# Kernel tuning notes

Measured on AMD Instinct MI355X. Metric: run time of the kernel, lower is better.

Reference implementation:

```python
import jax, jax.numpy as jnp
import numpy as np

L = 4          # GAT_LAYERS
HEADS = 4      # N_HEADS
H = 64         # transformer hidden dim
DH = H // HEADS
FIN = 32       # NODE_EMBED_SIZE
A = 15         # gats.num_actions (readout size)
OBS = 1500     # flattened obs dim
HS = 512       # hidden_size (policy FC)
NOUT = 15      # num_outputs
VH = 128       # VALUE_HIDDENS
B = 128        # batch of graphs
N = 1000       # nodes per map graph
TOT = B * N
DEG = 4
E = TOT * DEG


def _lin(key, fan_in, shape):
    return jax.random.normal(key, shape, jnp.float32) * (1.0 / np.sqrt(fan_in))


def setup_inputs() -> dict:
    key = jax.random.key(0)
    ks = jax.random.split(key, 30)
    node_feats = jax.random.normal(ks[0], (TOT, FIN), jnp.float32)
    obs = jax.random.normal(ks[1], (B, OBS), jnp.float32)
    # batched-graph edges: endpoints stay within each graph (DGL batch semantics)
    off = (jnp.arange(B) * N)[:, None]
    edge_src = (jax.random.randint(ks[2], (B, N * DEG), 0, N) + off).reshape(-1).astype(jnp.int32)
    edge_dst = (jax.random.randint(ks[3], (B, N * DEG), 0, N) + off).reshape(-1).astype(jnp.int32)
    agent_nodes = (jax.random.randint(ks[4], (B,), 0, N) + jnp.arange(B) * N).astype(jnp.int32)
    p = {
        'W_in': _lin(ks[5], FIN, (FIN, H)),
        'Wq': _lin(ks[6], H, (L, H, H)), 'Wk': _lin(ks[7], H, (L, H, H)),
        'Wv': _lin(ks[8], H, (L, H, H)), 'Wo': _lin(ks[9], H, (L, H, H)),
        'ln1_g': jnp.ones((L, H), jnp.float32), 'ln1_b': jnp.zeros((L, H), jnp.float32),
        'W1': _lin(ks[10], H, (L, H, 2 * H)), 'b1': jnp.zeros((L, 2 * H), jnp.float32),
        'W2': _lin(ks[11], 2 * H, (L, 2 * H, H)), 'b2': jnp.zeros((L, H), jnp.float32),
        'ln2_g': jnp.ones((L, H), jnp.float32), 'ln2_b': jnp.zeros((L, H), jnp.float32),
        'Wr': _lin(ks[12], H, (H, A)), 'br': jnp.zeros((A,), jnp.float32),
        'Wp1': _lin(ks[13], A + OBS, (A + OBS, HS)), 'bp1': jnp.zeros((HS,), jnp.float32),
        'Wp2': _lin(ks[14], HS, (HS, HS)), 'bp2': jnp.zeros((HS,), jnp.float32),
        'Wlog': _lin(ks[15], HS, (HS, NOUT)), 'blog': jnp.zeros((NOUT,), jnp.float32),
        'Wv1': _lin(ks[16], OBS, (OBS, VH)), 'bv1': jnp.zeros((VH,), jnp.float32),
        'Wv2': _lin(ks[17], VH, (VH, VH)), 'bv2': jnp.zeros((VH,), jnp.float32),
        'Wvo': _lin(ks[18], VH, (VH, 1)), 'bvo': jnp.zeros((1,), jnp.float32),
    }
    return dict(node_feats=node_feats, obs=obs, edge_src=edge_src, edge_dst=edge_dst,
                agent_nodes=agent_nodes, **p)


def _layernorm(x, g, b):
    m = x.mean(-1, keepdims=True)
    v = ((x - m) ** 2).mean(-1, keepdims=True)
    return (x - m) * jax.lax.rsqrt(v + 1e-5) * g + b


def reference(node_feats, obs, edge_src, edge_dst, agent_nodes, W_in, Wq, Wk, Wv, Wo,
              ln1_g, ln1_b, W1, b1, W2, b2, ln2_g, ln2_b, Wr, br,
              Wp1, bp1, Wp2, bp2, Wlog, blog, Wv1, bv1, Wv2, bv2, Wvo, bvo):
    n = node_feats.shape[0]
    x = node_feats @ W_in                                   # [n, H]
    inv_sqrt_dh = np.float32(1.0 / np.sqrt(DH))
    for l in range(L):
        q = (x @ Wq[l]).reshape(n, HEADS, DH)
        k = (x @ Wk[l]).reshape(n, HEADS, DH)
        v = (x @ Wv[l]).reshape(n, HEADS, DH)
        # per-edge attention scores, softmax over incoming edges of each dst node
        s = jnp.sum(q[edge_dst] * k[edge_src], axis=-1) * inv_sqrt_dh   # [E, HEADS]
        m = jax.ops.segment_max(s, edge_dst, num_segments=n)            # [n, HEADS]
        w = jnp.exp(s - m[edge_dst])
        denom = jax.ops.segment_sum(w, edge_dst, num_segments=n)        # [n, HEADS]
        agg = jax.ops.segment_sum(w[:, :, None] * v[edge_src], edge_dst, num_segments=n)
        attn = (agg / (denom[:, :, None] + 1e-9)).reshape(n, H) @ Wo[l]
        x = _layernorm(x + attn, ln1_g[l], ln1_b[l])
        h = jax.nn.relu(x @ W1[l] + b1[l]) @ W2[l] + b2[l]
        x = _layernorm(x + h, ln2_g[l], ln2_b[l])
    gat_out = x[agent_nodes] @ Wr + br                      # [B, A] per-agent action features
    feat = jnp.tanh(jnp.concatenate([gat_out, obs], axis=1) @ Wp1 + bp1)
    feat = jnp.tanh(feat @ Wp2 + bp2)
    logits = feat @ Wlog + blog                             # [B, NOUT]
    vh = jnp.tanh(obs @ Wv1 + bv1)
    vh = jnp.tanh(vh @ Wv2 + bv2)
    value = (vh @ Wvo + bvo)[:, 0]                          # [B]
    return logits, value
```

## Files before the change

kernel.cpp:

```cpp
#include <hip/hip_runtime.h>
#include <hip/hip_bf16.h>
#include <cstdint>
#include <cstddef>

#define DEV static __device__ __forceinline__

constexpr int GRAPHS = 128;
constexpr int NPG    = 1000;
constexpr int EPG    = 4000;
constexpr int TOTN   = GRAPHS * NPG;
constexpr int TOTE   = GRAPHS * EPG;
constexpr int HD     = 64;
constexpr int OBSD   = 1500;
constexpr int AD     = 15;

typedef __attribute__((ext_vector_type(8))) short bf16x8;
typedef __attribute__((ext_vector_type(4))) float f32x4;

DEV unsigned short f2b(float f){
  unsigned u = __float_as_uint(f);
  return (unsigned short)((u + 0x7fffu + ((u >> 16) & 1u)) >> 16);
}
DEV float b2f(unsigned short s){ return __uint_as_float((unsigned)s << 16); }

// ... 69 lines not shown
  int e = blockIdx.x*256 + threadIdx.x;
  int pos = atomicAdd(&cursor[edst[e]], 1);
  esorted[pos] = esrc[e];
}

__global__ __launch_bounds__(256) void k_in(const float* __restrict__ nf,
                                            const float* __restrict__ Win,
                                            unsigned short* __restrict__ xb){
  __shared__ float  s_nf[256*36];
  __shared__ float4 s_w[512];
  const int tid = threadIdx.x;
  const int node0 = blockIdx.x * 256;
  const float4* W4 = (const float4*)Win;
  s_w[tid] = W4[tid]; s_w[tid+256] = W4[tid+256];
  const float4* nf4 = (const float4*)nf;
  float4* snf4 = (float4*)s_nf;
  #pragma unroll
  for (int r=0;r<8;r++){
    int i = tid + 256*r; int n = i>>3, k4 = i&7;
    snf4[n*9 + k4] = nf4[(size_t)(node0+n)*8 + k4];
  }
  __syncthreads();
  const int ng = tid>>2, cg = tid&3;
  float4 acc[4][4];
  #pragma unroll
  for (int i=0;i<4;i++){ acc[i][0]=make_float4(0,0,0,0); acc[i][1]=make_float4(0,0,0,0);
                         acc[i][2]=make_float4(0,0,0,0); acc[i][3]=make_float4(0,0,0,0); }
  #pragma unroll 4
  for (int k=0;k<32;k++){
    float nv[4];
    #pragma unroll
    for (int i=0;i<4;i++) nv[i] = s_nf[(ng + 64*i)*36 + k];
    float4 w[4];
    #pragma unroll
    for (int j=0;j<4;j++) w[j] = s_w[k*16 + cg*4 + j];
    #pragma unroll
    for (int i=0;i<4;i++){
      #pragma unroll
      for (int j=0;j<4;j++) fma4(acc[i][j], nv[i], w[j]);
    }
  }
  ushort4* xb4 = (ushort4*)xb;
  #pragma unroll
  for (int i=0;i<4;i++){
    size_t nidx = (size_t)(node0 + ng + 64*i) * 16;
    #pragma unroll
    for (int j=0;j<4;j++) xb4[nidx + cg*4 + j] = pack4(acc[i][j]);
  }
}

__global__ __launch_bounds__(256) void k_qkv_m(const unsigned short* __restrict__ xb,
    const unsigned short* __restrict__ wqkvT,
    unsigned short* __restrict__ qkv){
  __shared__ short s_w[192*72];
  __shared__ short s_st[4][16*104];
  const int tid = threadIdx.x;
  const int node0 = blockIdx.x * 256;
  {
    const unsigned* src = (const unsigned*)wqkvT;
    unsigned* dst = (unsigned*)s_w;
    #pragma unroll
    for (int r=0;r<24;r++){
      int j = tid + 256*r;
      int c = j >> 5, kk = j & 31;
      dst[c*36 + kk] = src[j];
    }
  }
  __syncthreads();
  const int lane = tid & 63, wave = tid >> 6;
  const int m = lane & 15, quad = lane >> 4;
  const int rowbase = node0 + wave*64;
  bf16x8 af[4][2];
  #pragma unroll
  for (int rt=0;rt<4;rt++){
    const unsigned short* xp = xb + (size_t)(rowbase + rt*16 + m)*64 + quad*8;
    af[rt][0] = *(const bf16x8*)xp;
    af[rt][1] = *(const bf16x8*)(xp + 32);
  }
  short* st = s_st[wave];
  #pragma unroll
  for (int rt=0;rt<4;rt++){
    #pragma unroll
    for (int half=0; half<2; half++){
      #pragma unroll
      for (int c6=0;c6<6;c6++){
        int ct = half*6 + c6;
        bf16x8 b0 = *(const bf16x8*)&s_w[(ct*16+m)*72 + quad*8];
        bf16x8 b1 = *(const bf16x8*)&s_w[(ct*16+m)*72 + 32 + quad*8];
        f32x4 acc = {0.f,0.f,0.f,0.f};
        acc = __builtin_amdgcn_mfma_f32_16x16x32_bf16(af[rt][0], b0, acc, 0,0,0);
        acc = __builtin_amdgcn_mfma_f32_16x16x32_bf16(af[rt][1], b1, acc, 0,0,0);
        #pragma unroll
        for (int i=0;i<4;i++)
          st[(quad*4+i)*104 + c6*16 + m] = (short)f2b(acc[i]);
      }
      #pragma unroll
      for (int j=0;j<3;j++){
        int flat = (j*64 + lane)*8;
        int r = flat / 96, c = flat % 96;
        bf16x8 v = *(const bf16x8*)&st[r*104 + c];
        *(bf16x8*)(qkv + (size_t)(rowbase + rt*16 + r)*192 + half*96 + c) = v;
      }
    }
  }
}

__global__ __launch_bounds__(256) void k_edge2(const unsigned short* __restrict__ qkv,
    const int* __restrict__ rstart, const int* __restrict__ cnt,
    const int* __restrict__ esorted, unsigned short* __restrict__ attn_in){
  const int tid = threadIdx.x;
  const int wb = (blockIdx.x & 7)*1000 + (blockIdx.x >> 3);
  const int lane = tid & 63;
  const int sub  = lane >> 4;
  const int dg   = lane & 15;
  const int wave = tid >> 6;
  const int node = wb*16 + wave*4 + sub;
  const ushort4* row = (const ushort4*)(qkv + (size_t)node*192);
  ushort4 qu = row[dg];
  float q0 = b2f(qu.x), q1 = b2f(qu.y), q2 = b2f(qu.z), q3 = b2f(qu.w);
  const int rs = rstart[node];
  const int n  = cnt[node];
  float a0=0.f, a1=0.f, a2=0.f, a3=0.f, den=0.f;
  for (int i=0;i<n;i++){
    int src = esorted[rs + i];
    ushort4 ku = *(const ushort4*)(qkv + (size_t)src*192 + 64 + dg*4);
    ushort4 vu = *(const ushort4*)(qkv + (size_t)src*192 + 128 + dg*4);
    float p = q0*b2f(ku.x) + q1*b2f(ku.y) + q2*b2f(ku.z) + q3*b2f(ku.w);
    p += __shfl_xor(p, 1);
    p += __shfl_xor(p, 2);
    float w = __expf(p * 0.25f);
    den += w;
    a0 = fmaf(w, b2f(vu.x), a0);
    a1 = fmaf(w, b2f(vu.y), a1);
    a2 = fmaf(w, b2f(vu.z), a2);
    a3 = fmaf(w, b2f(vu.w), a3);
  }
  float inv = 1.0f/(den + 1e-9f);
  ushort4 o;
  o.x = f2b(a0*inv); o.y = f2b(a1*inv); o.z = f2b(a2*inv); o.w = f2b(a3*inv);
  ((ushort4*)attn_in)[(size_t)node*16 + dg] = o;
}

__global__ __launch_bounds__(256) void k_attn_m(const unsigned short* __restrict__ attn_in,
    const unsigned short* __restrict__ woT, const float* __restrict__ lg,
    const float* __restrict__ lb, unsigned short* __restrict__ xb){
  __shared__ short s_w[64*72];
  __shared__ short s_st[4][16*72];
  const int tid = threadIdx.x;
  const int node0 = blockIdx.x*256;
  {
    const unsigned* src = (const unsigned*)woT;
    unsigned* dst = (unsigned*)s_w;
    #pragma unroll
    for (int r=0;r<8;r++){
      int j = tid + 256*r;
      int c = j >> 5, kk = j & 31;
      dst[c*36 + kk] = src[j];
    }
  }
  __syncthreads();
  const int lane = tid&63, wave = tid>>6;
  const int m = lane&15, quad = lane>>4;
  const int rowbase = node0 + wave*64;
  bf16x8 bf[4][2];
  #pragma unroll
  for (int ct=0;ct<4;ct++){
    bf[ct][0] = *(const bf16x8*)&s_w[(ct*16+m)*72 + quad*8];
    bf[ct][1] = *(const bf16x8*)&s_w[(ct*16+m)*72 + 32 + quad*8];
  }
  float g[4], bb[4];
  #pragma unroll
  for (int ct=0;ct<4;ct++){ g[ct]=lg[ct*16+m]; bb[ct]=lb[ct*16+m]; }
  short* st = s_st[wave];
  #pragma unroll
  for (int rt=0;rt<4;rt++){
    const unsigned short* ap = attn_in + (size_t)(rowbase + rt*16 + m)*64 + quad*8;
    bf16x8 a0 = *(const bf16x8*)ap;
    bf16x8 a1 = *(const bf16x8*)(ap + 32);
    f32x4 acc[4];
    #pragma unroll
    for (int ct=0;ct<4;ct++){
      f32x4 z = {0.f,0.f,0.f,0.f};
      z = __builtin_amdgcn_mfma_f32_16x16x32_bf16(a0, bf[ct][0], z, 0,0,0);
      z = __builtin_amdgcn_mfma_f32_16x16x32_bf16(a1, bf[ct][1], z, 0,0,0);
      acc[ct] = z;
    }
    #pragma unroll
    for (int i=0;i<4;i++){
      size_t row = (size_t)(rowbase + rt*16 + quad*4 + i)*64;
      float v0 = acc[0][i] + b2f(xb[row + m]);
      float v1 = acc[1][i] + b2f(xb[row + 16 + m]);
      float v2 = acc[2][i] + b2f(xb[row + 32 + m]);
      float v3 = acc[3][i] + b2f(xb[row + 48 + m]);
      float sm = v0+v1+v2+v3;
      float sq = v0*v0+v1*v1+v2*v2+v3*v3;
      #pragma unroll
      for (int mk=1; mk<16; mk<<=1){ sm += __shfl_xor(sm, mk); sq += __shfl_xor(sq, mk); }
      float mean = sm*0.015625f;
      float var  = sq*0.015625f - mean*mean;
      float rs   = rsqrtf(var + 1e-5f);
      int rl = quad*4 + i;
      st[rl*72 + m]      = (short)f2b((v0-mean)*rs*g[0]+bb[0]);
      st[rl*72 + 16 + m] = (short)f2b((v1-mean)*rs*g[1]+bb[1]);
      st[rl*72 + 32 + m] = (short)f2b((v2-mean)*rs*g[2]+bb[2]);
      st[rl*72 + 48 + m] = (short)f2b((v3-mean)*rs*g[3]+bb[3]);
    }
    #pragma unroll
    for (int j=0;j<2;j++){
      int flat = (j*64 + lane)*8;
      int r = flat >> 6, c = flat & 63;
      bf16x8 v = *(const bf16x8*)&st[r*72 + c];
      *(bf16x8*)(xb + (size_t)(rowbase + rt*16 + r)*64 + c) = v;
    }
  }
}

__global__ __launch_bounds__(256) void k_ffn_m(unsigned short* __restrict__ xb,
    const unsigned short* __restrict__ w1T, const float* __restrict__ b1_l,
    const unsigned short* __restrict__ w2T, const float* __restrict__ b2_l,
    const float* __restrict__ lg, const float* __restrict__ lb){
  __shared__ short s_w1[128*72];
  __shared__ short s_w2[64*136];
  __shared__ short s_st[4][16*136];
  const int tid = threadIdx.x;
  const int node0 = blockIdx.x*256;
  {
    const unsigned* src = (const unsigned*)w1T;
    unsigned* dst = (unsigned*)s_w1;
    #pragma unroll
    for (int r=0;r<16;r++){
      int j = tid + 256*r;
      int c = j >> 5, kk = j & 31;
      dst[c*36 + kk] = src[j];
    }
  }
  {
    const unsigned* src = (const unsigned*)w2T;
    unsigned* dst = (unsigned*)s_w2;
    #pragma unroll
    for (int r=0;r<16;r++){
      int j = tid + 256*r;
      int c = j >> 6, kk = j & 63;
      dst[c*68 + kk] = src[j];
    }
  }
  __syncthreads();
  const int lane = tid&63, wave = tid>>6;
  const int m = lane&15, quad = lane>>4;
  const int rowbase = node0 + wave*64;
  bf16x8 af[4][2];
  #pragma unroll
  for (int rt=0;rt<4;rt++){
    const unsigned short* xp = xb + (size_t)(rowbase + rt*16 + m)*64 + quad*8;
    af[rt][0] = *(const bf16x8*)xp;
    af[rt][1] = *(const bf16x8*)(xp + 32);
  }
  float g[4], bb[4], b2v[4];
  #pragma unroll
  for (int ct=0;ct<4;ct++){ g[ct]=lg[ct*16+m]; bb[ct]=lb[ct*16+m]; b2v[ct]=b2_l[ct*16+m]; }
  short* st = s_st[wave];
  #pragma unroll
  for (int rt=0;rt<4;rt++){
    #pragma unroll
    for (int ct=0;ct<8;ct++){
      bf16x8 b0 = *(const bf16x8*)&s_w1[(ct*16+m)*72 + quad*8];
      bf16x8 b1 = *(const bf16x8*)&s_w1[(ct*16+m)*72 + 32 + quad*8];
      float bias = b1_l[ct*16+m];
      f32x4 acc = {0.f,0.f,0.f,0.f};
      acc = __builtin_amdgcn_mfma_f32_16x16x32_bf16(af[rt][0], b0, acc, 0,0,0);
      acc = __builtin_amdgcn_mfma_f32_16x16x32_bf16(af[rt][1], b1, acc, 0,0,0);
      #pragma unroll
      for (int i=0;i<4;i++)
        st[(quad*4+i)*136 + ct*16 + m] = (short)f2b(fmaxf(acc[i]+bias, 0.f));
    }
    bf16x8 h0 = *(const bf16x8*)&st[m*136 + quad*8];
    bf16x8 h1 = *(const bf16x8*)&st[m*136 + 32 + quad*8];
    bf16x8 h2 = *(const bf16x8*)&st[m*136 + 64 + quad*8];
    bf16x8 h3 = *(const bf16x8*)&st[m*136 + 96 + quad*8];
    f32x4 acc2[4];
    #pragma unroll
    for (int ct=0;ct<4;ct++){
      f32x4 z = {0.f,0.f,0.f,0.f};
      z = __builtin_amdgcn_mfma_f32_16x16x32_bf16(h0, *(const bf16x8*)&s_w2[(ct*16+m)*136 + quad*8],      z, 0,0,0);
      z = __builtin_amdgcn_mfma_f32_16x16x32_bf16(h1, *(const bf16x8*)&s_w2[(ct*16+m)*136 + 32 + quad*8], z, 0,0,0);
      z = __builtin_amdgcn_mfma_f32_16x16x32_bf16(h2, *(const bf16x8*)&s_w2[(ct*16+m)*136 + 64 + quad*8], z, 0,0,0);
      z = __builtin_amdgcn_mfma_f32_16x16x32_bf16(h3, *(const bf16x8*)&s_w2[(ct*16+m)*136 + 96 + quad*8], z, 0,0,0);
      acc2[ct] = z;
    }
    #pragma unroll
    for (int i=0;i<4;i++){
      size_t row = (size_t)(rowbase + rt*16 + quad*4 + i)*64;
      float v0 = acc2[0][i] + b2v[0] + b2f(xb[row + m]);
      float v1 = acc2[1][i] + b2v[1] + b2f(xb[row + 16 + m]);
      float v2 = acc2[2][i] + b2v[2] + b2f(xb[row + 32 + m]);
      float v3 = acc2[3][i] + b2v[3] + b2f(xb[row + 48 + m]);
      float sm = v0+v1+v2+v3;
      float sq = v0*v0+v1*v1+v2*v2+v3*v3;
      #pragma unroll
      for (int mk=1; mk<16; mk<<=1){ sm += __shfl_xor(sm, mk); sq += __shfl_xor(sq, mk); }
      float mean = sm*0.015625f;
      float var  = sq*0.015625f - mean*mean;
      float rs   = rsqrtf(var + 1e-5f);
      int rl = quad*4 + i;
      st[rl*136 + m]      = (short)f2b((v0-mean)*rs*g[0]+bb[0]);
      st[rl*136 + 16 + m] = (short)f2b((v1-mean)*rs*g[1]+bb[1]);
      st[rl*136 + 32 + m] = (short)f2b((v2-mean)*rs*g[2]+bb[2]);
      st[rl*136 + 48 + m] = (short)f2b((v3-mean)*rs*g[3]+bb[3]);
    }
    #pragma unroll
    for (int j=0;j<2;j++){
      int flat = (j*64 + lane)*8;
      int r = flat >> 6, c = flat & 63;
      bf16x8 v = *(const bf16x8*)&st[r*136 + c];
      *(bf16x8*)(xb + (size_t)(rowbase + rt*16 + r)*64 + c) = v;
    }
  }
}

__global__ __launch_bounds__(256) void k_feat(const unsigned short* __restrict__ xb,
    const float* __restrict__ obs, const int* __restrict__ agents,
    const float* __restrict__ Wr, const float* __restrict__ br,
    float* __restrict__ feat){
  __shared__ float s_xa[64];
  const int b = blockIdx.x, tid = threadIdx.x;
  if (tid < 64) s_xa[tid] = b2f(xb[(size_t)agents[b]*HD + tid]);
  __syncthreads();
  if (tid < AD){
    float a = br[tid];
    #pragma unroll 8
    for (int k=0;k<HD;k++) a = fmaf(s_xa[k], Wr[k*AD + tid], a);
    feat[(size_t)b*1536 + tid] = a;
  }
  for (int i=tid;i<OBSD;i+=256) feat[(size_t)b*1536 + AD + i] = obs[(size_t)b*OBSD + i];
  if (tid < 21) feat[(size_t)b*1536 + 1515 + tid] = 0.f;
}

template<int ROWS, int COLS, int CH, int KS, int N>
__global__ __launch_bounds__(ROWS*COLS) void k_gemm_part(
    const float* __restrict__ A, int lda, int K,
    const float* __restrict__ W, float* __restrict__ part){
  constexpr int BT = ROWS*COLS;
  __shared__ float s_a[ROWS*CH];
  const int tid = threadIdx.x;
  const int ct = blockIdx.x, rg = blockIdx.y, ks = blockIdx.z;
  const int chunk = (K + KS - 1) / KS;
  const int k0 = ks * chunk;
  const int len = min(K - k0, chunk);
  const int row0 = rg * ROWS;
  #pragma unroll
  for (int rr=0; rr<ROWS; rr++)
    for (int i=tid; i<len; i+=BT)
      s_a[rr*CH + i] = A[(size_t)(row0+rr)*lda + k0 + i];
  __syncthreads();
  const int r = tid / COLS, c = tid % COLS;
  const float* wp = W + (size_t)k0*N + ct*COLS + c;
  const float* ap = s_a + r*CH;
  float acc = 0.f;
  #pragma unroll 8
  for (int k=0;k<len;k++) acc = fmaf(ap[k], wp[(size_t)k*N], acc);
  part[((size_t)ks*128 + row0 + r)*N + ct*COLS + c] = acc;
}

template<int KS, int N, bool TANH>
__global__ __launch_bounds__(256) void k_reduce(const float* __restrict__ part,
    const float* __restrict__ bias, float* __restrict__ out, int MN){
  const int idx = blockIdx.x*256 + threadIdx.x;
  if (idx >= MN) return;
  float s = bias[idx & (N-1)];
// ... 58 lines not shown
  const int*   esrc   = (const int*)d_in[2];
  const int*   edst   = (const int*)d_in[3];
  const int*   agents = (const int*)d_in[4];
  const float* Win    = (const float*)d_in[5];
  const float* Wq     = (const float*)d_in[6];
  const float* Wk     = (const float*)d_in[7];
  const float* Wv     = (const float*)d_in[8];
  const float* Wo     = (const float*)d_in[9];
  const float* ln1g   = (const float*)d_in[10];
  const float* ln1b   = (const float*)d_in[11];
  const float* W1     = (const float*)d_in[12];
  const float* b1     = (const float*)d_in[13];
  const float* W2     = (const float*)d_in[14];
  const float* b2     = (const float*)d_in[15];
  const float* ln2g   = (const float*)d_in[16];
  const float* ln2b   = (const float*)d_in[17];
  const float* Wr     = (const float*)d_in[18];
  const float* br     = (const float*)d_in[19];
  const float* Wp1    = (const float*)d_in[20];
  const float* bp1    = (const float*)d_in[21];
  const float* Wp2    = (const float*)d_in[22];
  const float* bp2    = (const float*)d_in[23];
  const float* Wlog   = (const float*)d_in[24];
  const float* blog   = (const float*)d_in[25];
  const float* Wv1    = (const float*)d_in[26];
  const float* bv1    = (const float*)d_in[27];
  const float* Wv2    = (const float*)d_in[28];
  const float* bv2    = (const float*)d_in[29];
  const float* Wvo    = (const float*)d_in[30];
  const float* bvo    = (const float*)d_in[31];
  float* out = (float*)d_out;

  unsigned short* xb      = (unsigned short*)d_ws;
  unsigned short* qkv     = xb + (size_t)TOTN*HD;
  unsigned short* attn_in = qkv + (size_t)TOTN*192;
  unsigned short* wpack   = attn_in + (size_t)TOTN*HD;
  int* cnt     = (int*)(wpack + 131072);
  int* rstart  = cnt + TOTN;
  int* cursor  = rstart + TOTN;
  int* esorted = cursor + TOTN;
  float* feat = (float*)(esorted + TOTE);
  float* f1   = feat + 128*1536;
  float* f2   = f1 + 128*512;
  float* vh   = f2 + 128*512;
  float* part = vh + 128*128;

  k_wprep  <<<512, 256, 0, stream>>>(Wq, Wk, Wv, Wo, W1, W2, wpack);
  k_zero   <<<TOTN/256, 256, 0, stream>>>(cnt);
  k_hist   <<<TOTE/256, 256, 0, stream>>>(edst, cnt);
  k_scan   <<<GRAPHS, 1024, 0, stream>>>(cnt, rstart, cursor);
  k_scatter<<<TOTE/256, 256, 0, stream>>>(esrc, edst, cursor, esorted);

  k_in<<<TOTN/256, 256, 0, stream>>>(nf, Win, xb);
  for (int l=0; l<4; l++){
    const unsigned short* wl = wpack + l*32768;
    k_qkv_m <<<TOTN/256, 256, 0, stream>>>(xb, wl, qkv);
    k_edge2 <<<TOTN/16, 256, 0, stream>>>(qkv, rstart, cnt, esorted, attn_in);
    k_attn_m<<<TOTN/256, 256, 0, stream>>>(attn_in, wl + 12288,
                                           ln1g + l*64, ln1b + l*64, xb);
    k_ffn_m <<<TOTN/256, 256, 0, stream>>>(xb, wl + 16384, b1 + l*128,
                                           wl + 24576, b2 + l*64,
                                           ln2g + l*64, ln2b + l*64);
  }
  k_feat<<<GRAPHS, 256, 0, stream>>>(xb, obs, agents, Wr, br, feat);
  k_gemm_part<2,256,384,4,512><<<dim3(2,64,4), 512, 0, stream>>>(feat, 1536, 1515, Wp1, part);
  k_reduce<4,512,true><<<256, 256, 0, stream>>>(part, bp1, f1, 128*512);
  k_gemm_part<2,256,256,2,512><<<dim3(2,64,2), 512, 0, stream>>>(f1, 512, 512, Wp2, part);
  k_reduce<2,512,true><<<256, 256, 0, stream>>>(part, bp2, f2, 128*512);
  k_logits<<<GRAPHS, 256, 0, stream>>>(f2, Wlog, blog, out);
  k_gemm_part<4,128,192,8,128><<<dim3(1,32,8), 512, 0, stream>>>(obs, 1500, 1500, Wv1, part);
  k_reduce<8,128,true><<<64, 256, 0, stream>>>(part, bv1, vh, 128*128);
  k_vfin<<<GRAPHS, 128, 0, stream>>>(vh, Wv2, bv2, Wvo, bvo, out);
}
```

Measured before the change: 534.5 us.

## Fuse Wo, FFN, layernorms and next-layer QKV into one per-layer node kernel

Merges the attention output projection, first layernorm, FFN, second layernorm and the next layer's QKV projection into a single k_node kernel. Intermediate activations stay in per-wave LDS instead of round-tripping through global memory, which removes two launches and several xb reads and writes per layer. Weight staging into shared memory is also dropped; MFMA B-operands are read straight from global memory and rely on the cache. This lowers LDS use but can raise global load latency per MFMA.

```diff
diff --git a/kernel.cpp b/kernel.cpp
--- a/kernel.cpp
+++ b/kernel.cpp
@@ -145,21 +145,9 @@
 __global__ __launch_bounds__(256) void k_qkv_m(const unsigned short* __restrict__ xb,
     const unsigned short* __restrict__ wqkvT,
     unsigned short* __restrict__ qkv){
-  __shared__ short s_w[192*72];
   __shared__ short s_st[4][16*104];
   const int tid = threadIdx.x;
   const int node0 = blockIdx.x * 256;
-  {
-    const unsigned* src = (const unsigned*)wqkvT;
-    unsigned* dst = (unsigned*)s_w;
-    #pragma unroll
-    for (int r=0;r<24;r++){
-      int j = tid + 256*r;
-      int c = j >> 5, kk = j & 31;
-      dst[c*36 + kk] = src[j];
-    }
-  }
-  __syncthreads();
   const int lane = tid & 63, wave = tid >> 6;
   const int m = lane & 15, quad = lane >> 4;
   const int rowbase = node0 + wave*64;
@@ -178,8 +166,8 @@
       #pragma unroll
       for (int c6=0;c6<6;c6++){
         int ct = half*6 + c6;
-        bf16x8 b0 = *(const bf16x8*)&s_w[(ct*16+m)*72 + quad*8];
-        bf16x8 b1 = *(const bf16x8*)&s_w[(ct*16+m)*72 + 32 + quad*8];
+        bf16x8 b0 = *(const bf16x8*)&wqkvT[(ct*16+m)*64 + quad*8];
+        bf16x8 b1 = *(const bf16x8*)&wqkvT[(ct*16+m)*64 + 32 + quad*8];
         f32x4 acc = {0.f,0.f,0.f,0.f};
         acc = __builtin_amdgcn_mfma_f32_16x16x32_bf16(af[rt][0], b0, acc, 0,0,0);
         acc = __builtin_amdgcn_mfma_f32_16x16x32_bf16(af[rt][1], b1, acc, 0,0,0);
@@ -234,37 +222,43 @@
   ((ushort4*)attn_in)[(size_t)node*16 + dg] = o;
 }
 
-__global__ __launch_bounds__(256) void k_attn_m(const unsigned short* __restrict__ attn_in,
-    const unsigned short* __restrict__ woT, const float* __restrict__ lg,
-    const float* __restrict__ lb, unsigned short* __restrict__ xb){
-  __shared__ short s_w[64*72];
-  __shared__ short s_st[4][16*72];
+__global__ __launch_bounds__(256) void k_node(
+    const unsigned short* __restrict__ attn_in,
+    unsigned short* __restrict__ xb,
+    const unsigned short* __restrict__ woT,
+    const unsigned short* __restrict__ w1T,
+    const float* __restrict__ b1_l,
+    const unsigned short* __restrict__ w2T,
+    const float* __restrict__ b2_l,
+    const float* __restrict__ l1g, const float* __restrict__ l1b,
+    const float* __restrict__ l2g, const float* __restrict__ l2b,
+    const unsigned short* __restrict__ wqkvT,
+    unsigned short* __restrict__ qkv){
+  __shared__ short s_x1[4][16*72];
+  __shared__ short s_h[4][16*136];
   const int tid = threadIdx.x;
   const int node0 = blockIdx.x*256;
-  {
-    const unsigned* src = (const unsigned*)woT;
-    unsigned* dst = (unsigned*)s_w;
-    #pragma unroll
-    for (int r=0;r<8;r++){
-      int j = tid + 256*r;
-      int c = j >> 5, kk = j & 31;
-      dst[c*36 + kk] = src[j];
-    }
-  }
-  __syncthreads();
   const int lane = tid&63, wave = tid>>6;
   const int m = lane&15, quad = lane>>4;
   const int rowbase = node0 + wave*64;
-  bf16x8 bf[4][2];
+  bf16x8 wo[4][2];
   #pragma unroll
   for (int ct=0;ct<4;ct++){
-    bf[ct][0] = *(const bf16x8*)&s_w[(ct*16+m)*72 + quad*8];
-    bf[ct][1] = *(const bf16x8*)&s_w[(ct*16+m)*72 + 32 + quad*8];
-  }
-  float g[4], bb[4];
-  #pragma unroll
-  for (int ct=0;ct<4;ct++){ g[ct]=lg[ct*16+m]; bb[ct]=lb[ct*16+m]; }
-  short* st = s_st[wave];
+    wo[ct][0] = *(const bf16x8*)&woT[(ct*16+m)*64 + quad*8];
+    wo[ct][1] = *(const bf16x8*)&woT[(ct*16+m)*64 + 32 + quad*8];
+  }
+  float g1[4], bb1[4], g2[4], bb2[4], b2v[4];
+  #pragma unroll
+  for (int ct=0;ct<4;ct++){
+    g1[ct]=l1g[ct*16+m]; bb1[ct]=l1b[ct*16+m];
+    g2[ct]=l2g[ct*16+m]; bb2[ct]=l2b[ct*16+m];
+    b2v[ct]=b2_l[ct*16+m];
+  }
+  float b1v[8];
+  #pragma unroll
+  for (int ct=0;ct<8;ct++) b1v[ct]=b1_l[ct*16+m];
+  short* sx = s_x1[wave];
+  short* sh = s_h[wave];
   #pragma unroll
   for (int rt=0;rt<4;rt++){
     const unsigned short* ap = attn_in + (size_t)(rowbase + rt*16 + m)*64 + quad*8;
@@ -274,8 +268,8 @@
     #pragma unroll
     for (int ct=0;ct<4;ct++){
       f32x4 z = {0.f,0.f,0.f,0.f};
-      z = __builtin_amdgcn_mfma_f32_16x16x32_bf16(a0, bf[ct][0], z, 0,0,0);
-      z = __builtin_amdgcn_mfma_f32_16x16x32_bf16(a1, bf[ct][1], z, 0,0,0);
+      z = __builtin_amdgcn_mfma_f32_16x16x32_bf16(a0, wo[ct][0], z, 0,0,0);
+      z = __builtin_amdgcn_mfma_f32_16x16x32_bf16(a1, wo[ct][1], z, 0,0,0);
       acc[ct] = z;
     }
     #pragma unroll
@@ -293,100 +287,45 @@
       float var  = sq*0.015625f - mean*mean;
       float rs   = rsqrtf(var + 1e-5f);
       int rl = quad*4 + i;
-      st[rl*72 + m]      = (short)f2b((v0-mean)*rs*g[0]+bb[0]);
-      st[rl*72 + 16 + m] = (short)f2b((v1-mean)*rs*g[1]+bb[1]);
-      st[rl*72 + 32 + m] = (short)f2b((v2-mean)*rs*g[2]+bb[2]);
-      st[rl*72 + 48 + m] = (short)f2b((v3-mean)*rs*g[3]+bb[3]);
-    }
-    #pragma unroll
-    for (int j=0;j<2;j++){
-      int flat = (j*64 + lane)*8;
-      int r = flat >> 6, c = flat & 63;
-      bf16x8 v = *(const bf16x8*)&st[r*72 + c];
-      *(bf16x8*)(xb + (size_t)(rowbase + rt*16 + r)*64 + c) = v;
-    }
-  }
-}
-
-__global__ __launch_bounds__(256) void k_ffn_m(unsigned short* __restrict__ xb,
-    const unsigned short* __restrict__ w1T, const float* __restrict__ b1_l,
-    const unsigned short* __restrict__ w2T, const float* __restrict__ b2_l,
-    const float* __restrict__ lg, const float* __restrict__ lb){
-  __shared__ short s_w1[128*72];
-  __shared__ short s_w2[64*136];
-  __shared__ short s_st[4][16*136];
-  const int tid = threadIdx.x;
-  const int node0 = blockIdx.x*256;
-  {
-    const unsigned* src = (const unsigned*)w1T;
-    unsigned* dst = (unsigned*)s_w1;
-    #pragma unroll
-    for (int r=0;r<16;r++){
-      int j = tid + 256*r;
-      int c = j >> 5, kk = j & 31;
-      dst[c*36 + kk] = src[j];
-    }
-  }
-  {
-    const unsigned* src = (const unsigned*)w2T;
-    unsigned* dst = (unsigned*)s_w2;
-    #pragma unroll
-    for (int r=0;r<16;r++){
-      int j = tid + 256*r;
-      int c = j >> 6, kk = j & 63;
-      dst[c*68 + kk] = src[j];
-    }
-  }
-  __syncthreads();
-  const int lane = tid&63, wave = tid>>6;
-  const int m = lane&15, quad = lane>>4;
-  const int rowbase = node0 + wave*64;
-  bf16x8 af[4][2];
-  #pragma unroll
-  for (int rt=0;rt<4;rt++){
-    const unsigned short* xp = xb + (size_t)(rowbase + rt*16 + m)*64 + quad*8;
-    af[rt][0] = *(const bf16x8*)xp;
-    af[rt][1] = *(const bf16x8*)(xp + 32);
-  }
-  float g[4], bb[4], b2v[4];
-  #pragma unroll
-  for (int ct=0;ct<4;ct++){ g[ct]=lg[ct*16+m]; bb[ct]=lb[ct*16+m]; b2v[ct]=b2_l[ct*16+m]; }
-  short* st = s_st[wave];
-  #pragma unroll
-  for (int rt=0;rt<4;rt++){
+      sx[rl*72 + m]      = (short)f2b((v0-mean)*rs*g1[0]+bb1[0]);
+      sx[rl*72 + 16 + m] = (short)f2b((v1-mean)*rs*g1[1]+bb1[1]);
+      sx[rl*72 + 32 + m] = (short)f2b((v2-mean)*rs*g1[2]+bb1[2]);
+      sx[rl*72 + 48 + m] = (short)f2b((v3-mean)*rs*g1[3]+bb1[3]);
+    }
+    bf16x8 x10 = *(const bf16x8*)&sx[m*72 + quad*8];
+    bf16x8 x11 = *(const bf16x8*)&sx[m*72 + 32 + quad*8];
     #pragma unroll
     for (int ct=0;ct<8;ct++){
-      bf16x8 b0 = *(const bf16x8*)&s_w1[(ct*16+m)*72 + quad*8];
-      bf16x8 b1 = *(const bf16x8*)&s_w1[(ct*16+m)*72 + 32 + quad*8];
-      float bias = b1_l[ct*16+m];
-      f32x4 acc = {0.f,0.f,0.f,0.f};
-      acc = __builtin_amdgcn_mfma_f32_16x16x32_bf16(af[rt][0], b0, acc, 0,0,0);
-      acc = __builtin_amdgcn_mfma_f32_16x16x32_bf16(af[rt][1], b1, acc, 0,0,0);
+      bf16x8 b0 = *(const bf16x8*)&w1T[(ct*16+m)*64 + quad*8];
+      bf16x8 b1f = *(const bf16x8*)&w1T[(ct*16+m)*64 + 32 + quad*8];
+      f32x4 z = {0.f,0.f,0.f,0.f};
+      z = __builtin_amdgcn_mfma_f32_16x16x32_bf16(x10, b0, z, 0,0,0);
+      z = __builtin_amdgcn_mfma_f32_16x16x32_bf16(x11, b1f, z, 0,0,0);
       #pragma unroll
       for (int i=0;i<4;i++)
-        st[(quad*4+i)*136 + ct*16 + m] = (short)f2b(fmaxf(acc[i]+bias, 0.f));
-    }
-    bf16x8 h0 = *(const bf16x8*)&st[m*136 + quad*8];
-    bf16x8 h1 = *(const bf16x8*)&st[m*136 + 32 + quad*8];
-    bf16x8 h2 = *(const bf16x8*)&st[m*136 + 64 + quad*8];
-    bf16x8 h3 = *(const bf16x8*)&st[m*136 + 96 + quad*8];
+        sh[(quad*4+i)*136 + ct*16 + m] = (short)f2b(fmaxf(z[i]+b1v[ct], 0.f));
+    }
+    bf16x8 h0 = *(const bf16x8*)&sh[m*136 + quad*8];
+    bf16x8 h1 = *(const bf16x8*)&sh[m*136 + 32 + quad*8];
+    bf16x8 h2 = *(const bf16x8*)&sh[m*136 + 64 + quad*8];
+    bf16x8 h3 = *(const bf16x8*)&sh[m*136 + 96 + quad*8];
     f32x4 acc2[4];
     #pragma unroll
     for (int ct=0;ct<4;ct++){
       f32x4 z = {0.f,0.f,0.f,0.f};
-      z = __builtin_amdgcn_mfma_f32_16x16x32_bf16(h0, *(const bf16x8*)&s_w2[(ct*16+m)*136 + quad*8],      z, 0,0,0);
-      z = __builtin_amdgcn_mfma_f32_16x16x32_bf16(h1, *(const bf16x8*)&s_w2[(ct*16+m)*136 + 32 + quad*8], z, 0,0,0);
-      z = __builtin_amdgcn_mfma_f32_16x16x32_bf16(h2, *(const bf16x8*)&s_w2[(ct*16+m)*136 + 64 + quad*8], z, 0,0,0);
-      z = __builtin_amdgcn_mfma_f32_16x16x32_bf16(h3, *(const bf16x8*)&s_w2[(ct*16+m)*136 + 96 + quad*8], z, 0,0,0);
+      z = __builtin_amdgcn_mfma_f32_16x16x32_bf16(h0, *(const bf16x8*)&w2T[(ct*16+m)*128 + quad*8],      z, 0,0,0);
+      z = __builtin_amdgcn_mfma_f32_16x16x32_bf16(h1, *(const bf16x8*)&w2T[(ct*16+m)*128 + 32 + quad*8], z, 0,0,0);
+      z = __builtin_amdgcn_mfma_f32_16x16x32_bf16(h2, *(const bf16x8*)&w2T[(ct*16+m)*128 + 64 + quad*8], z, 0,0,0);
+      z = __builtin_amdgcn_mfma_f32_16x16x32_bf16(h3, *(const bf16x8*)&w2T[(ct*16+m)*128 + 96 + quad*8], z, 0,0,0);
       acc2[ct] = z;
     }
     #pragma unroll
     for (int i=0;i<4;i++){
-      size_t row = (size_t)(rowbase + rt*16 + quad*4 + i)*64;
-      float v0 = acc2[0][i] + b2v[0] + b2f(xb[row + m]);
-      float v1 = acc2[1][i] + b2v[1] + b2f(xb[row + 16 + m]);
-      float v2 = acc2[2][i] + b2v[2] + b2f(xb[row + 32 + m]);
-      float v3 = acc2[3][i] + b2v[3] + b2f(xb[row + 48 + m]);
+      int rl = quad*4 + i;
+      float v0 = acc2[0][i] + b2v[0] + b2f((unsigned short)sx[rl*72 + m]);
+      float v1 = acc2[1][i] + b2v[1] + b2f((unsigned short)sx[rl*72 + 16 + m]);
+      float v2 = acc2[2][i] + b2v[2] + b2f((unsigned short)sx[rl*72 + 32 + m]);
+      float v3 = acc2[3][i] + b2v[3] + b2f((unsigned short)sx[rl*72 + 48 + m]);
       float sm = v0+v1+v2+v3;
       float sq = v0*v0+v1*v1+v2*v2+v3*v3;
       #pragma unroll
@@ -394,18 +333,43 @@
       float mean = sm*0.015625f;
       float var  = sq*0.015625f - mean*mean;
       float rs   = rsqrtf(var + 1e-5f);
-      int rl = quad*4 + i;
-      st[rl*136 + m]      = (short)f2b((v0-mean)*rs*g[0]+bb[0]);
-      st[rl*136 + 16 + m] = (short)f2b((v1-mean)*rs*g[1]+bb[1]);
-      st[rl*136 + 32 + m] = (short)f2b((v2-mean)*rs*g[2]+bb[2]);
-      st[rl*136 + 48 + m] = (short)f2b((v3-mean)*rs*g[3]+bb[3]);
+      sx[rl*72 + m]      = (short)f2b((v0-mean)*rs*g2[0]+bb2[0]);
+      sx[rl*72 + 16 + m] = (short)f2b((v1-mean)*rs*g2[1]+bb2[1]);
+      sx[rl*72 + 32 + m] = (short)f2b((v2-mean)*rs*g2[2]+bb2[2]);
+      sx[rl*72 + 48 + m] = (short)f2b((v3-mean)*rs*g2[3]+bb2[3]);
     }
     #pragma unroll
     for (int j=0;j<2;j++){
       int flat = (j*64 + lane)*8;
       int r = flat >> 6, c = flat & 63;
-      bf16x8 v = *(const bf16x8*)&st[r*136 + c];
+      bf16x8 v = *(const bf16x8*)&sx[r*72 + c];
       *(bf16x8*)(xb + (size_t)(rowbase + rt*16 + r)*64 + c) = v;
+    }
+    if (wqkvT){
+      bf16x8 q0 = *(const bf16x8*)&sx[m*72 + quad*8];
+      bf16x8 q1 = *(const bf16x8*)&sx[m*72 + 32 + quad*8];
+      #pragma unroll
+      for (int half=0; half<2; half++){
+        #pragma unroll
+        for (int c6=0;c6<6;c6++){
+          int ct = half*6 + c6;
+          bf16x8 b0 = *(const bf16x8*)&wqkvT[(ct*16+m)*64 + quad*8];
+          bf16x8 b1f = *(const bf16x8*)&wqkvT[(ct*16+m)*64 + 32 + quad*8];
+          f32x4 z = {0.f,0.f,0.f,0.f};
+          z = __builtin_amdgcn_mfma_f32_16x16x32_bf16(q0, b0, z, 0,0,0);
+          z = __builtin_amdgcn_mfma_f32_16x16x32_bf16(q1, b1f, z, 0,0,0);
+          #pragma unroll
+          for (int i=0;i<4;i++)
+            sh[(quad*4+i)*136 + c6*16 + m] = (short)f2b(z[i]);
+        }
+        #pragma unroll
+        for (int j=0;j<3;j++){
+          int flat = (j*64 + lane)*8;
+          int r = flat / 96, c = flat % 96;
+          bf16x8 v = *(const bf16x8*)&sh[r*136 + c];
+          *(bf16x8*)(qkv + (size_t)(rowbase + rt*16 + r)*192 + half*96 + c) = v;
+        }
+      }
     }
   }
 }
@@ -571,15 +535,18 @@
   k_scatter<<<TOTE/256, 256, 0, stream>>>(esrc, edst, cursor, esorted);
 
   k_in<<<TOTN/256, 256, 0, stream>>>(nf, Win, xb);
+  k_qkv_m<<<TOTN/256, 256, 0, stream>>>(xb, wpack, qkv);
   for (int l=0; l<4; l++){
     const unsigned short* wl = wpack + l*32768;
-    k_qkv_m <<<TOTN/256, 256, 0, stream>>>(xb, wl, qkv);
-    k_edge2 <<<TOTN/16, 256, 0, stream>>>(qkv, rstart, cnt, esorted, attn_in);
-    k_attn_m<<<TOTN/256, 256, 0, stream>>>(attn_in, wl + 12288,
-                                           ln1g + l*64, ln1b + l*64, xb);
-    k_ffn_m <<<TOTN/256, 256, 0, stream>>>(xb, wl + 16384, b1 + l*128,
-                                           wl + 24576, b2 + l*64,
-                                           ln2g + l*64, ln2b + l*64);
+    const unsigned short* wqkv_next = (l<3) ? (wpack + (l+1)*32768) : nullptr;
+    k_edge2<<<TOTN/16, 256, 0, stream>>>(qkv, rstart, cnt, esorted, attn_in);
+    k_node <<<TOTN/256, 256, 0, stream>>>(attn_in, xb,
+                                          wl + 12288,
+                                          wl + 16384, b1 + l*128,
+                                          wl + 24576, b2 + l*64,
+                                          ln1g + l*64, ln1b + l*64,
+                                          ln2g + l*64, ln2b + l*64,
+                                          wqkv_next, qkv);
   }
   k_feat<<<GRAPHS, 256, 0, stream>>>(xb, obs, agents, Wr, br, feat);
   k_gemm_part<2,256,384,4,512><<<dim3(2,64,4), 512, 0, stream>>>(feat, 1536, 1515, Wp1, part);
```

After: 617.0 us. 1.15x slower.

## Read weights directly from global memory and shrink per-block node tiles

Applied to the files above, without the earlier changes.

The three per-node MFMA kernels (QKV, attention output projection, FFN) no longer stage weight matrices into LDS behind a block barrier. Each wave now reads its B fragments straight from global memory, where the small weights should stay cache-resident, and handles 16 nodes instead of 64. Launch grids grow fourfold. This removes the LDS fill and __syncthreads and frees shared memory for higher occupancy, at the cost of repeated global and cache weight reads and more blocks.

```diff
diff --git a/kernel.cpp b/kernel.cpp
--- a/kernel.cpp
+++ b/kernel.cpp
@@ -145,55 +145,35 @@
 __global__ __launch_bounds__(256) void k_qkv_m(const unsigned short* __restrict__ xb,
     const unsigned short* __restrict__ wqkvT,
     unsigned short* __restrict__ qkv){
-  __shared__ short s_w[192*72];
   __shared__ short s_st[4][16*104];
   const int tid = threadIdx.x;
-  const int node0 = blockIdx.x * 256;
-  {
-    const unsigned* src = (const unsigned*)wqkvT;
-    unsigned* dst = (unsigned*)s_w;
-    #pragma unroll
-    for (int r=0;r<24;r++){
-      int j = tid + 256*r;
-      int c = j >> 5, kk = j & 31;
-      dst[c*36 + kk] = src[j];
-    }
-  }
-  __syncthreads();
   const int lane = tid & 63, wave = tid >> 6;
   const int m = lane & 15, quad = lane >> 4;
-  const int rowbase = node0 + wave*64;
-  bf16x8 af[4][2];
-  #pragma unroll
-  for (int rt=0;rt<4;rt++){
-    const unsigned short* xp = xb + (size_t)(rowbase + rt*16 + m)*64 + quad*8;
-    af[rt][0] = *(const bf16x8*)xp;
-    af[rt][1] = *(const bf16x8*)(xp + 32);
-  }
+  const int rowbase = blockIdx.x*64 + wave*16;
+  const unsigned short* xp = xb + (size_t)(rowbase + m)*64 + quad*8;
+  bf16x8 a0 = *(const bf16x8*)xp;
+  bf16x8 a1 = *(const bf16x8*)(xp + 32);
   short* st = s_st[wave];
   #pragma unroll
-  for (int rt=0;rt<4;rt++){
-    #pragma unroll
-    for (int half=0; half<2; half++){
+  for (int half=0; half<2; half++){
+    #pragma unroll
+    for (int c6=0;c6<6;c6++){
+      int ct = half*6 + c6;
+      bf16x8 b0 = *(const bf16x8*)&wqkvT[(ct*16+m)*64 + quad*8];
+      bf16x8 b1 = *(const bf16x8*)&wqkvT[(ct*16+m)*64 + 32 + quad*8];
+      f32x4 acc = {0.f,0.f,0.f,0.f};
+      acc = __builtin_amdgcn_mfma_f32_16x16x32_bf16(a0, b0, acc, 0,0,0);
+      acc = __builtin_amdgcn_mfma_f32_16x16x32_bf16(a1, b1, acc, 0,0,0);
       #pragma unroll
-      for (int c6=0;c6<6;c6++){
-        int ct = half*6 + c6;
-        bf16x8 b0 = *(const bf16x8*)&s_w[(ct*16+m)*72 + quad*8];
-        bf16x8 b1 = *(const bf16x8*)&s_w[(ct*16+m)*72 + 32 + quad*8];
-        f32x4 acc = {0.f,0.f,0.f,0.f};
-        acc = __builtin_amdgcn_mfma_f32_16x16x32_bf16(af[rt][0], b0, acc, 0,0,0);
-        acc = __builtin_amdgcn_mfma_f32_16x16x32_bf16(af[rt][1], b1, acc, 0,0,0);
-        #pragma unroll
-        for (int i=0;i<4;i++)
-          st[(quad*4+i)*104 + c6*16 + m] = (short)f2b(acc[i]);
-      }
-      #pragma unroll
-      for (int j=0;j<3;j++){
-        int flat = (j*64 + lane)*8;
-        int r = flat / 96, c = flat % 96;
-        bf16x8 v = *(const bf16x8*)&st[r*104 + c];
-        *(bf16x8*)(qkv + (size_t)(rowbase + rt*16 + r)*192 + half*96 + c) = v;
-      }
+      for (int i=0;i<4;i++)
+        st[(quad*4+i)*104 + c6*16 + m] = (short)f2b(acc[i]);
+    }
+    #pragma unroll
+    for (int j=0;j<3;j++){
+      int flat = (j*64 + lane)*8;
+      int r = flat / 96, c = flat % 96;
+      bf16x8 v = *(const bf16x8*)&st[r*104 + c];
+      *(bf16x8*)(qkv + (size_t)(rowbase + r)*192 + half*96 + c) = v;
     }
   }
 }
@@ -237,74 +217,58 @@
 __global__ __launch_bounds__(256) void k_attn_m(const unsigned short* __restrict__ attn_in,
     const unsigned short* __restrict__ woT, const float* __restrict__ lg,
     const float* __restrict__ lb, unsigned short* __restrict__ xb){
-  __shared__ short s_w[64*72];
   __shared__ short s_st[4][16*72];
   const int tid = threadIdx.x;
-  const int node0 = blockIdx.x*256;
-  {
-    const unsigned* src = (const unsigned*)woT;
-    unsigned* dst = (unsigned*)s_w;
-    #pragma unroll
-    for (int r=0;r<8;r++){
-      int j = tid + 256*r;
-      int c = j >> 5, kk = j & 31;
-      dst[c*36 + kk] = src[j];
-    }
-  }
-  __syncthreads();
   const int lane = tid&63, wave = tid>>6;
   const int m = lane&15, quad = lane>>4;
-  const int rowbase = node0 + wave*64;
-  bf16x8 bf[4][2];
+  const int rowbase = blockIdx.x*64 + wave*16;
+  bf16x8 wo[4][2];
   #pragma unroll
   for (int ct=0;ct<4;ct++){
-    bf[ct][0] = *(const bf16x8*)&s_w[(ct*16+m)*72 + quad*8];
-    bf[ct][1] = *(const bf16x8*)&s_w[(ct*16+m)*72 + 32 + quad*8];
+    wo[ct][0] = *(const bf16x8*)&woT[(ct*16+m)*64 + quad*8];
+    wo[ct][1] = *(const bf16x8*)&woT[(ct*16+m)*64 + 32 + quad*8];
   }
   float g[4], bb[4];
   #pragma unroll
   for (int ct=0;ct<4;ct++){ g[ct]=lg[ct*16+m]; bb[ct]=lb[ct*16+m]; }
   short* st = s_st[wave];
-  #pragma unroll
-  for (int rt=0;rt<4;rt++){
-    const unsigned short* ap = attn_in + (size_t)(rowbase + rt*16 + m)*64 + quad*8;
-    bf16x8 a0 = *(const bf16x8*)ap;
-    bf16x8 a1 = *(const bf16x8*)(ap + 32);
-    f32x4 acc[4];
-    #pragma unroll
-    for (int ct=0;ct<4;ct++){
-      f32x4 z = {0.f,0.f,0.f,0.f};
-      z = __builtin_amdgcn_mfma_f32_16x16x32_bf16(a0, bf[ct][0], z, 0,0,0);
-      z = __builtin_amdgcn_mfma_f32_16x16x32_bf16(a1, bf[ct][1], z, 0,0,0);
-      acc[ct] = z;
-    }
-    #pragma unroll
-    for (int i=0;i<4;i++){
-      size_t row = (size_t)(rowbase + rt*16 + quad*4 + i)*64;
-      float v0 = acc[0][i] + b2f(xb[row + m]);
-      float v1 = acc[1][i] + b2f(xb[row + 16 + m]);
-      float v2 = acc[2][i] + b2f(xb[row + 32 + m]);
-      float v3 = acc[3][i] + b2f(xb[row + 48 + m]);
-      float sm = v0+v1+v2+v3;
-      float sq = v0*v0+v1*v1+v2*v2+v3*v3;
-      #pragma unroll
-      for (int mk=1; mk<16; mk<<=1){ sm += __shfl_xor(sm, mk); sq += __shfl_xor(sq, mk); }
-      float mean = sm*0.015625f;
-      float var  = sq*0.015625f - mean*mean;
-      float rs   = rsqrtf(var + 1e-5f);
-      int rl = quad*4 + i;
-      st[rl*72 + m]      = (short)f2b((v0-mean)*rs*g[0]+bb[0]);
-      st[rl*72 + 16 + m] = (short)f2b((v1-mean)*rs*g[1]+bb[1]);
-      st[rl*72 + 32 + m] = (short)f2b((v2-mean)*rs*g[2]+bb[2]);
-      st[rl*72 + 48 + m] = (short)f2b((v3-mean)*rs*g[3]+bb[3]);
-    }
-    #pragma unroll
-    for (int j=0;j<2;j++){
-      int flat = (j*64 + lane)*8;
-      int r = flat >> 6, c = flat & 63;
-      bf16x8 v = *(const bf16x8*)&st[r*72 + c];
-      *(bf16x8*)(xb + (size_t)(rowbase + rt*16 + r)*64 + c) = v;
-    }
+  const unsigned short* ap = attn_in + (size_t)(rowbase + m)*64 + quad*8;
+  bf16x8 a0 = *(const bf16x8*)ap;
+  bf16x8 a1 = *(const bf16x8*)(ap + 32);
+  f32x4 acc[4];
+  #pragma unroll
+  for (int ct=0;ct<4;ct++){
+    f32x4 z = {0.f,0.f,0.f,0.f};
+    z = __builtin_amdgcn_mfma_f32_16x16x32_bf16(a0, wo[ct][0], z, 0,0,0);
+    z = __builtin_amdgcn_mfma_f32_16x16x32_bf16(a1, wo[ct][1], z, 0,0,0);
+    acc[ct] = z;
+  }
+  #pragma unroll
+  for (int i=0;i<4;i++){
+    size_t row = (size_t)(rowbase + quad*4 + i)*64;
+    float v0 = acc[0][i] + b2f(xb[row + m]);
+    float v1 = acc[1][i] + b2f(xb[row + 16 + m]);
+    float v2 = acc[2][i] + b2f(xb[row + 32 + m]);
+    float v3 = acc[3][i] + b2f(xb[row + 48 + m]);
+    float sm = v0+v1+v2+v3;
+    float sq = v0*v0+v1*v1+v2*v2+v3*v3;
+    #pragma unroll
+    for (int mk=1; mk<16; mk<<=1){ sm += __shfl_xor(sm, mk); sq += __shfl_xor(sq, mk); }
+    float mean = sm*0.015625f;
+    float var  = sq*0.015625f - mean*mean;
+    float rs   = rsqrtf(var + 1e-5f);
+    int rl = quad*4 + i;
+    st[rl*72 + m]      = (short)f2b((v0-mean)*rs*g[0]+bb[0]);
+    st[rl*72 + 16 + m] = (short)f2b((v1-mean)*rs*g[1]+bb[1]);
+    st[rl*72 + 32 + m] = (short)f2b((v2-mean)*rs*g[2]+bb[2]);
+    st[rl*72 + 48 + m] = (short)f2b((v3-mean)*rs*g[3]+bb[3]);
+  }
+  #pragma unroll
+  for (int j=0;j<2;j++){
+    int flat = (j*64 + lane)*8;
+    int r = flat >> 6, c = flat & 63;
+    bf16x8 v = *(const bf16x8*)&st[r*72 + c];
+    *(bf16x8*)(xb + (size_t)(rowbase + r)*64 + c) = v;
   }
 }
 
@@ -312,101 +276,70 @@
     const unsigned short* __restrict__ w1T, const float* __restrict__ b1_l,
     const unsigned short* __restrict__ w2T, const float* __restrict__ b2_l,
     const float* __restrict__ lg, const float* __restrict__ lb){
-  __shared__ short s_w1[128*72];
-  __shared__ short s_w2[64*136];
   __shared__ short s_st[4][16*136];
   const int tid = threadIdx.x;
-  const int node0 = blockIdx.x*256;
-  {
-    const unsigned* src = (const unsigned*)w1T;
-    unsigned* dst = (unsigned*)s_w1;
-    #pragma unroll
-    for (int r=0;r<16;r++){
-      int j = tid + 256*r;
-      int c = j >> 5, kk = j & 31;
-      dst[c*36 + kk] = src[j];
-    }
-  }
-  {
-    const unsigned* src = (const unsigned*)w2T;
-    unsigned* dst = (unsigned*)s_w2;
-    #pragma unroll
-    for (int r=0;r<16;r++){
-      int j = tid + 256*r;
-      int c = j >> 6, kk = j & 63;
-      dst[c*68 + kk] = src[j];
-    }
-  }
-  __syncthreads();
   const int lane = tid&63, wave = tid>>6;
   const int m = lane&15, quad = lane>>4;
-  const int rowbase = node0 + wave*64;
-  bf16x8 af[4][2];
-  #pragma unroll
-  for (int rt=0;rt<4;rt++){
-    const unsigned short* xp = xb + (size_t)(rowbase + rt*16 + m)*64 + quad*8;
-    af[rt][0] = *(const bf16x8*)xp;
-    af[rt][1] = *(const bf16x8*)(xp + 32);
-  }
+  const int rowbase = blockIdx.x*64 + wave*16;
+  const unsigned short* xp = xb + (size_t)(rowbase + m)*64 + quad*8;
+  bf16x8 a0 = *(const bf16x8*)xp;
+  bf16x8 a1 = *(const bf16x8*)(xp + 32);
   float g[4], bb[4], b2v[4];
   #pragma unroll
   for (int ct=0;ct<4;ct++){ g[ct]=lg[ct*16+m]; bb[ct]=lb[ct*16+m]; b2v[ct]=b2_l[ct*16+m]; }
   short* st = s_st[wave];
   #pragma unroll
-  for (int rt=0;rt<4;rt++){
-    #pragma unroll
-    for (int ct=0;ct<8;ct++){
-      bf16x8 b0 = *(const bf16x8*)&s_w1[(ct*16+m)*72 + quad*8];
-      bf16x8 b1 = *(const bf16x8*)&s_w1[(ct*16+m)*72 + 32 + quad*8];
-      float bias = b1_l[ct*16+m];
-      f32x4 acc = {0.f,0.f,0.f,0.f};
-      acc = __builtin_amdgcn_mfma_f32_16x16x32_bf16(af[rt][0], b0, acc, 0,0,0);
-      acc = __builtin_amdgcn_mfma_f32_16x16x32_bf16(af[rt][1], b1, acc, 0,0,0);
-      #pragma unroll
-      for (int i=0;i<4;i++)
-        st[(quad*4+i)*136 + ct*16 + m] = (short)f2b(fmaxf(acc[i]+bias, 0.f));
-    }
-    bf16x8 h0 = *(const bf16x8*)&st[m*136 + quad*8];
-    bf16x8 h1 = *(const bf16x8*)&st[m*136 + 32 + quad*8];
-    bf16x8 h2 = *(const bf16x8*)&st[m*136 + 64 + quad*8];
-    bf16x8 h3 = *(const bf16x8*)&st[m*136 + 96 + quad*8];
-    f32x4 acc2[4];
-    #pragma unroll
-    for (int ct=0;ct<4;ct++){
-      f32x4 z = {0.f,0.f,0.f,0.f};
-      z = __builtin_amdgcn_mfma_f32_16x16x32_bf16(h0, *(const bf16x8*)&s_w2[(ct*16+m)*136 + quad*8],      z, 0,0,0);
-      z = __builtin_amdgcn_mfma_f32_16x16x32_bf16(h1, *(const bf16x8*)&s_w2[(ct*16+m)*136 + 32 + quad*8], z, 0,0,0);
-      z = __builtin_amdgcn_mfma_f32_16x16x32_bf16(h2, *(const bf16x8*)&s_w2[(ct*16+m)*136 + 64 + quad*8], z, 0,0,0);
-      z = __builtin_amdgcn_mfma_f32_16x16x32_bf16(h3, *(const bf16x8*)&s_w2[(ct*16+m)*136 + 96 + quad*8], z, 0,0,0);
-      acc2[ct] = z;
-    }
-    #pragma unroll
-    for (int i=0;i<4;i++){
-      size_t row = (size_t)(rowbase + rt*16 + quad*4 + i)*64;
-      float v0 = acc2[0][i] + b2v[0] + b2f(xb[row + m]);
-      float v1 = acc2[1][i] + b2v[1] + b2f(xb[row + 16 + m]);
-      float v2 = acc2[2][i] + b2v[2] + b2f(xb[row + 32 + m]);
-      float v3 = acc2[3][i] + b2v[3] + b2f(xb[row + 48 + m]);
-      float sm = v0+v1+v2+v3;
-      float sq = v0*v0+v1*v1+v2*v2+v3*v3;
-      #pragma unroll
-      for (int mk=1; mk<16; mk<<=1){ sm += __shfl_xor(sm, mk); sq += __shfl_xor(sq, mk); }
-      float mean = sm*0.015625f;
-      float var  = sq*0.015625f - mean*mean;
-      float rs   = rsqrtf(var + 1e-5f);
-      int rl = quad*4 + i;
-      st[rl*136 + m]      = (short)f2b((v0-mean)*rs*g[0]+bb[0]);
-      st[rl*136 + 16 + m] = (short)f2b((v1-mean)*rs*g[1]+bb[1]);
-      st[rl*136 + 32 + m] = (short)f2b((v2-mean)*rs*g[2]+bb[2]);
-      st[rl*136 + 48 + m] = (short)f2b((v3-mean)*rs*g[3]+bb[3]);
-    }
-    #pragma unroll
-    for (int j=0;j<2;j++){
-      int flat = (j*64 + lane)*8;
-      int r = flat >> 6, c = flat & 63;
-      bf16x8 v = *(const bf16x8*)&st[r*136 + c];
-      *(bf16x8*)(xb + (size_t)(rowbase + rt*16 + r)*64 + c) = v;
-    }
+  for (int ct=0;ct<8;ct++){
+    bf16x8 b0 = *(const bf16x8*)&w1T[(ct*16+m)*64 + quad*8];
+    bf16x8 b1 = *(const bf16x8*)&w1T[(ct*16+m)*64 + 32 + quad*8];
+    float bias = b1_l[ct*16+m];
+    f32x4 acc = {0.f,0.f,0.f,0.f};
+    acc = __builtin_amdgcn_mfma_f32_16x16x32_bf16(a0, b0, acc, 0,0,0);
+    acc = __builtin_amdgcn_mfma_f32_16x16x32_bf16(a1, b1, acc, 0,0,0);
+    #pragma unroll
+    for (int i=0;i<4;i++)
+      st[(quad*4+i)*136 + ct*16 + m] = (short)f2b(fmaxf(acc[i]+bias, 0.f));
+  }
+  bf16x8 h0 = *(const bf16x8*)&st[m*136 + quad*8];
+  bf16x8 h1 = *(const bf16x8*)&st[m*136 + 32 + quad*8];
+  bf16x8 h2 = *(const bf16x8*)&st[m*136 + 64 + quad*8];
+  bf16x8 h3 = *(const bf16x8*)&st[m*136 + 96 + quad*8];
+  f32x4 acc2[4];
+  #pragma unroll
+  for (int ct=0;ct<4;ct++){
+    f32x4 z = {0.f,0.f,0.f,0.f};
+    z = __builtin_amdgcn_mfma_f32_16x16x32_bf16(h0, *(const bf16x8*)&w2T[(ct*16+m)*128 + quad*8],      z, 0,0,0);
+    z = __builtin_amdgcn_mfma_f32_16x16x32_bf16(h1, *(const bf16x8*)&w2T[(ct*16+m)*128 + 32 + quad*8], z, 0,0,0);
+    z = __builtin_amdgcn_mfma_f32_16x16x32_bf16(h2, *(const bf16x8*)&w2T[(ct*16+m)*128 + 64 + quad*8], z, 0,0,0);
+    z = __builtin_amdgcn_mfma_f32_16x16x32_bf16(h3, *(const bf16x8*)&w2T[(ct*16+m)*128 + 96 + quad*8], z, 0,0,0);
+    acc2[ct] = z;
+  }
+  #pragma unroll
+  for (int i=0;i<4;i++){
+    size_t row = (size_t)(rowbase + quad*4 + i)*64;
+    float v0 = acc2[0][i] + b2v[0] + b2f(xb[row + m]);
+    float v1 = acc2[1][i] + b2v[1] + b2f(xb[row + 16 + m]);
+    float v2 = acc2[2][i] + b2v[2] + b2f(xb[row + 32 + m]);
+    float v3 = acc2[3][i] + b2v[3] + b2f(xb[row + 48 + m]);
+    float sm = v0+v1+v2+v3;
+    float sq = v0*v0+v1*v1+v2*v2+v3*v3;
+    #pragma unroll
+    for (int mk=1; mk<16; mk<<=1){ sm += __shfl_xor(sm, mk); sq += __shfl_xor(sq, mk); }
+    float mean = sm*0.015625f;
+    float var  = sq*0.015625f - mean*mean;
+    float rs   = rsqrtf(var + 1e-5f);
+    int rl = quad*4 + i;
+    st[rl*136 + m]      = (short)f2b((v0-mean)*rs*g[0]+bb[0]);
+    st[rl*136 + 16 + m] = (short)f2b((v1-mean)*rs*g[1]+bb[1]);
+    st[rl*136 + 32 + m] = (short)f2b((v2-mean)*rs*g[2]+bb[2]);
+    st[rl*136 + 48 + m] = (short)f2b((v3-mean)*rs*g[3]+bb[3]);
+  }
+  #pragma unroll
+  for (int j=0;j<2;j++){
+    int flat = (j*64 + lane)*8;
+    int r = flat >> 6, c = flat & 63;
+    bf16x8 v = *(const bf16x8*)&st[r*136 + c];
+    *(bf16x8*)(xb + (size_t)(rowbase + r)*64 + c) = v;
   }
 }
 
@@ -573,13 +506,13 @@
   k_in<<<TOTN/256, 256, 0, stream>>>(nf, Win, xb);
   for (int l=0; l<4; l++){
     const unsigned short* wl = wpack + l*32768;
-    k_qkv_m <<<TOTN/256, 256, 0, stream>>>(xb, wl, qkv);
+    k_qkv_m <<<TOTN/64, 256, 0, stream>>>(xb, wl, qkv);
     k_edge2 <<<TOTN/16, 256, 0, stream>>>(qkv, rstart, cnt, esorted, attn_in);
-    k_attn_m<<<TOTN/256, 256, 0, stream>>>(attn_in, wl + 12288,
-                                           ln1g + l*64, ln1b + l*64, xb);
-    k_ffn_m <<<TOTN/256, 256, 0, stream>>>(xb, wl + 16384, b1 + l*128,
-                                           wl + 24576, b2 + l*64,
-                                           ln2g + l*64, ln2b + l*64);
+    k_attn_m<<<TOTN/64, 256, 0, stream>>>(attn_in, wl + 12288,
+                                          ln1g + l*64, ln1b + l*64, xb);
+    k_ffn_m <<<TOTN/64, 256, 0, stream>>>(xb, wl + 16384, b1 + l*128,
+                                          wl + 24576, b2 + l*64,
+                                          ln2g + l*64, ln2b + l*64);
   }
   k_feat<<<GRAPHS, 256, 0, stream>>>(xb, obs, agents, Wr, br, feat);
   k_gemm_part<2,256,384,4,512><<<dim3(2,64,4), 512, 0, stream>>>(feat, 1536, 1515, Wp1, part);
```

New measurement: 667.6 us. 24.9% more time.
